# Kernel tuning notes

Measured on AMD Instinct MI355X. Metric: run time of the kernel, lower is better.

The kernel has to match this reference:

```python
import jax, jax.numpy as jnp
import numpy as np

N_E = 1024
E_DIM = 256
N_TOK = 131072


def setup_inputs() -> dict:
    key = jax.random.key(0)
    kz, kw = jax.random.split(key)
    z = jax.random.normal(kz, (N_TOK, E_DIM), dtype=jnp.float32)
    weight = jax.random.normal(kw, (N_E, E_DIM), dtype=jnp.float32)
    return {"z": z, "weight": weight}


def reference(z, weight):
    # squared L2 distances: ||z||^2 + ||e||^2 - 2 z e^T  -> [N, n_e]
    d = (jnp.sum(z * z, axis=1, keepdims=True)
         + jnp.sum(weight * weight, axis=1)
         - 2.0 * jnp.matmul(z, weight.T))
    idx = jnp.argmin(d, axis=1)                       # [N]
    # gather codebook rows instead of materializing the one-hot @ weight matmul
    z_q = weight[idx]                                 # [N, e_dim]
    # straight-through estimator
    z_q = z + jax.lax.stop_gradient(z_q - z)
    # e_mean = mean of one-hot encodings == normalized code counts
    counts = jax.ops.segment_sum(jnp.ones_like(idx, dtype=z.dtype), idx,
                                 num_segments=N_E)    # [n_e]
    e_mean = counts / z.shape[0]
    perplexity = jnp.exp(-jnp.sum(e_mean * jnp.log(e_mean + 1e-10)))
    return z_q, perplexity
```

## Files before the change

### kernel.cpp

```cpp
#include <hip/hip_runtime.h>
#include <math.h>

#define NE   1024
#define ED   256
#define NT   131072
#define SLOTS 32

#define THR_REL 0.016f
#define THR_ABS 0.02f

typedef __attribute__((ext_vector_type(8))) short short8;
typedef __attribute__((ext_vector_type(4))) float f32x4;

__device__ inline unsigned short f2bf(float f) {
    unsigned u = __float_as_uint(f);
    unsigned r = (u + 0x7FFFu + ((u >> 16) & 1u)) >> 16;
    return (unsigned short)r;
}

__device__ inline void gl_lds16(const void* g, void* l) {
    __builtin_amdgcn_global_load_lds(
        (const __attribute__((address_space(1))) unsigned int*)g,
        (__attribute__((address_space(3))) unsigned int*)l, 16, 0, 0);
}

__device__ inline unsigned pack_cand(float s, int code) {
    float qf = (s + 1024.f) * 16.f;
    int q = (int)qf;
    q = q < 0 ? 0 : (q > 65535 ? 65535 : q);
    return ((unsigned)q << 16) | (unsigned)code;
}


__global__ __launch_bounds__(256) void vq_prep(const float* __restrict__ w,
                                               float* __restrict__ wnorm,
                                               int* __restrict__ counts,
                                               unsigned short* __restrict__ wb) {
    int c = blockIdx.x * 256 + threadIdx.x;
    if (c < NE) {
        const float4* row = reinterpret_cast<const float4*>(w + (size_t)c * ED);
        ushort4* wbr = reinterpret_cast<ushort4*>(wb + (size_t)c * ED);
        float s = 0.f;
#pragma unroll 8
        for (int i = 0; i < ED / 4; ++i) {
            float4 v = row[i];
            s += v.x * v.x + v.y * v.y + v.z * v.z + v.w * v.w;
            ushort4 o;
            o.x = f2bf(-2.f * v.x); o.y = f2bf(-2.f * v.y);
            o.z = f2bf(-2.f * v.z); o.w = f2bf(-2.f * v.w);
            wbr[i] = o;
        }
        wnorm[c] = s;
        counts[c] = 0;
    }
}

__global__ __launch_bounds__(1024) void vq_wmax(const float* __restrict__ wnorm,
                                                float* __restrict__ wmax) {
    __shared__ float red[16];
    int tid = threadIdx.x;
    float v = wnorm[tid];
#pragma unroll
    for (int m = 32; m >= 1; m >>= 1) v = fmaxf(v, __shfl_xor(v, m, 64));
    if ((tid & 63) == 0) red[tid >> 6] = v;
    __syncthreads();
    if (tid == 0) {
        float m = red[0];
#pragma unroll
        for (int i = 1; i < 16; ++i) m = fmaxf(m, red[i]);
        wmax[0] = sqrtf(m);
    }
}

__global__ __launch_bounds__(256) void vq_score8(const float* __restrict__ z,
                                                 const unsigned short* __restrict__ wb,
                                                 const float* __restrict__ wnorm,
                                                 const float* __restrict__ wmaxp,
                                                 unsigned* __restrict__ cnt,
                                                 unsigned* __restrict__ cand) {
    __shared__ __align__(16) unsigned short wlds[2][16384];
    __shared__ float wn_lds[NE];
    __shared__ float thr_lds[4][32];

    const int tid  = threadIdx.x;
    const int lane = tid & 63;
    const int wv_  = tid >> 6;
    const int l15  = lane & 15;
    const int l4   = lane >> 4;
    const int row0 = blockIdx.x * 128 + wv_ * 32;

#pragma unroll
    for (int p = 0; p < 8; ++p) {
        int s  = wv_ * 8 + p;
        int nj = s >> 3, kg = s & 7;
        gl_lds16(wb + (size_t)(nj * 16 + l15) * ED + kg * 32 + l4 * 8,
                 &wlds[0][s * 512]);
    }
#pragma unroll
    for (int p = 0; p < 8; ++p) {
        int s  = wv_ * 8 + p;
        int nj = s >> 3, kg = s & 7;
        gl_lds16(wb + (size_t)(64 + nj * 16 + l15) * ED + kg * 32 + l4 * 8,
                 &wlds[1][s * 512]);
    }

    reinterpret_cast<float4*>(wn_lds)[tid] = reinterpret_cast<const float4*>(wnorm)[tid];

    short8 a[2][8];
    float zn2[2];
#pragma unroll
    for (int mi = 0; mi < 2; ++mi) {
        const float* zr = z + (size_t)(row0 + mi * 16 + l15) * ED;
        float s = 0.f;
#pragma unroll
        for (int kg = 0; kg < 8; ++kg) {
            int k0 = kg * 32 + l4 * 8;
            float4 p = *reinterpret_cast<const float4*>(zr + k0);
            float4 q = *reinterpret_cast<const float4*>(zr + k0 + 4);
            s += p.x * p.x + p.y * p.y + p.z * p.z + p.w * p.w
               + q.x * q.x + q.y * q.y + q.z * q.z + q.w * q.w;
            short8 t;
            t[0] = (short)f2bf(p.x); t[1] = (short)f2bf(p.y);
            t[2] = (short)f2bf(p.z); t[3] = (short)f2bf(p.w);
            t[4] = (short)f2bf(q.x); t[5] = (short)f2bf(q.y);
            t[6] = (short)f2bf(q.z); t[7] = (short)f2bf(q.w);
            a[mi][kg] = t;
        }
        zn2[mi] = s;
    }
#pragma unroll
    for (int mi = 0; mi < 2; ++mi) {
        zn2[mi] += __shfl_xor(zn2[mi], 16, 64);
        zn2[mi] += __shfl_xor(zn2[mi], 32, 64);
    }
    float wmax = wmaxp[0];
#pragma unroll
    for (int mi = 0; mi < 2; ++mi)
        thr_lds[wv_][mi * 16 + l15] = THR_REL * sqrtf(zn2[mi]) * wmax + THR_ABS;

    asm volatile("s_waitcnt vmcnt(0) lgkmcnt(0)" ::: "memory");
    __builtin_amdgcn_s_barrier();

    float thrR[2], mn[2];
    int cnt_reg[2];
#pragma unroll
    for (int mi = 0; mi < 2; ++mi) {
        thrR[mi] = thr_lds[wv_][mi * 16 + l15];
        mn[mi] = 3.4e38f;
        cnt_reg[mi] = 0;
    }

    for (int st = 0; st < 16; ++st) {
        const int b  = st & 1;
        const int c0 = st * 64;

        if (st < 15) {
            asm volatile("s_waitcnt vmcnt(8)" ::: "memory");
        } else {
            asm volatile("s_waitcnt vmcnt(0)" ::: "memory");
        }
        __builtin_amdgcn_s_barrier();

        for (int base = 0; base < 4; base += 2) {
            f32x4 acc[2][2];
#pragma unroll
            for (int tb = 0; tb < 2; ++tb) {
                float4 wnv = *reinterpret_cast<const float4*>(
                    &wn_lds[c0 + (base + tb) * 16 + l4 * 4]);
                acc[tb][0] = {wnv.x, wnv.y, wnv.z, wnv.w};
                acc[tb][1] = {wnv.x, wnv.y, wnv.z, wnv.w};
            }

#pragma unroll
            for (int tb = 0; tb < 2; ++tb)
#pragma unroll
                for (int kg = 0; kg < 8; ++kg) {
                    short8 wf = *reinterpret_cast<const short8*>(
                        &wlds[b][(((base + tb) * 8 + kg) * 512) + lane * 8]);
                    acc[tb][0] = __builtin_amdgcn_mfma_f32_16x16x32_bf16(wf, a[0][kg], acc[tb][0], 0, 0, 0);
                    acc[tb][1] = __builtin_amdgcn_mfma_f32_16x16x32_bf16(wf, a[1][kg], acc[tb][1], 0, 0, 0);
                }

            float tmin[2] = {3.4e38f, 3.4e38f};
#pragma unroll
            for (int tb = 0; tb < 2; ++tb)
#pragma unroll
                for (int mi = 0; mi < 2; ++mi)
#pragma unroll
                    for (int r = 0; r < 4; ++r)
                        tmin[mi] = fminf(tmin[mi], acc[tb][mi][r]);
#pragma unroll
            for (int mi = 0; mi < 2; ++mi) {
                float v = tmin[mi];
                v = fminf(v, __shfl_xor(v, 16, 64));
                v = fminf(v, __shfl_xor(v, 32, 64));
                mn[mi] = fminf(mn[mi], v);
            }

            unsigned km[2] = {0u, 0u};
#pragma unroll
            for (int tb = 0; tb < 2; ++tb)
#pragma unroll
                for (int mi = 0; mi < 2; ++mi)
#pragma unroll
                    for (int r = 0; r < 4; ++r)
                        if (acc[tb][mi][r] <= mn[mi] + thrR[mi])
                            km[mi] |= 1u << (tb * 4 + r);

            if (__any((km[0] | km[1]) != 0u)) {
#pragma unroll
                for (int mi = 0; mi < 2; ++mi) {
                    int kc = __popc(km[mi]);
                    int b2 = __shfl_xor(kc, 16, 64);
                    int c2 = __shfl_xor(kc, 32, 64);
                    int d2 = __shfl_xor(b2, 32, 64);
                    int tot = kc + b2 + c2 + d2;
                    if (tot > 0) {
                        int pfx = (l4 == 1) ? b2
                                : (l4 == 2) ? (c2 + d2)
                                : (l4 == 3) ? (b2 + c2 + d2) : 0;
                        int tok = row0 + mi * 16 + l15;
                        int o = 0;
#pragma unroll
                        for (int tb = 0; tb < 2; ++tb)
#pragma unroll
                            for (int r = 0; r < 4; ++r)
                                if (km[mi] & (1u << (tb * 4 + r))) {
                                    int pos = cnt_reg[mi] + pfx + o;
                                    if (pos < SLOTS)
                                        cand[(size_t)tok * SLOTS + pos] =
                                            pack_cand(acc[tb][mi][r],
                                                      c0 + (base + tb) * 16 + l4 * 4 + r);
                                    ++o;
                                }
                        cnt_reg[mi] += tot;
                    }
                }
            }
        }

        asm volatile("s_waitcnt lgkmcnt(0)" ::: "memory");
        __builtin_amdgcn_s_barrier();
        if (st + 2 < 16) {
            const int cN = (st + 2) * 64;
#pragma unroll
            for (int p = 0; p < 8; ++p) {
                int s  = wv_ * 8 + p;
                int nj = s >> 3, kg = s & 7;
                gl_lds16(wb + (size_t)(cN + nj * 16 + l15) * ED + kg * 32 + l4 * 8,
                         &wlds[b][s * 512]);
            }
        }
    }

    if (l4 == 0) {
#pragma unroll
        for (int mi = 0; mi < 2; ++mi) {
            unsigned n = (unsigned)cnt_reg[mi];
            if (n > 255u) n = 255u;
            unsigned marg = (unsigned)(16.f * thrR[mi]) + 2u;
            cnt[row0 + mi * 16 + l15] = n | (marg << 8);
        }
    }
}

__global__ __launch_bounds__(256) void vq_refine(const float* __restrict__ z,
                                                 const float* __restrict__ w,
                                                 const float* __restrict__ wnorm,
                                                 const unsigned* __restrict__ cnt,
                                                 const unsigned* __restrict__ cand,
                                                 int* __restrict__ counts,
                                                 float* __restrict__ out) {
    const int lane = threadIdx.x & 63;
    const int t = blockIdx.x * 4 + (threadIdx.x >> 6);

    const unsigned tpack = cnt[t];
    const unsigned n     = tpack & 0xFFu;
    const unsigned margin = tpack >> 8;

    int bj = NE;
    bool need_exact = true;
    unsigned pk = 0xFFFFFFFFu;
    unsigned long long mask = 0ull;

    if (n >= 1u && n <= (unsigned)SLOTS) {
        if (lane < (int)n) pk = cand[(size_t)t * SLOTS + lane];
        unsigned pmin = pk;
#pragma unroll
        for (int m = 1; m < 64; m <<= 1) {
            unsigned o = __shfl_xor(pmin, m, 64);
            pmin = o < pmin ? o : pmin;
        }
        unsigned qmin = pmin >> 16;
        bool keep = (lane < (int)n) && ((pk >> 16) <= qmin + margin);
        mask = __ballot(keep);
        if (__popcll(mask) == 1) {
            int c = __ffsll(mask) - 1;
            bj = (int)(__shfl(pk, c, 64) & 0xFFFFu);
            need_exact = false;
        }
    }

    if (need_exact) {
        float4 zv = reinterpret_cast<const float4*>(z + (size_t)t * ED)[lane];
        float bs = 3.4e38f;
        bj = NE;
        if (n >= 1u && n <= (unsigned)SLOTS) {
            unsigned long long m2 = mask;
            while (m2) {
                int c = __ffsll(m2) - 1;
                m2 &= m2 - 1;
                int j = (int)(__shfl(pk, c, 64) & 0xFFFFu);
                float4 wv = reinterpret_cast<const float4*>(w + (size_t)j * ED)[lane];
                float d = fmaf(zv.x, wv.x, fmaf(zv.y, wv.y, fmaf(zv.z, wv.z, zv.w * wv.w)));
#pragma unroll
                for (int m = 1; m < 64; m <<= 1) d += __shfl_xor(d, m, 64);
                float s = fmaf(-2.f, d, wnorm[j]);
                if (s < bs || (s == bs && j < bj)) { bs = s; bj = j; }
            }
        } else {
            for (int j = 0; j < NE; ++j) {
                float4 wv = reinterpret_cast<const float4*>(w + (size_t)j * ED)[lane];
                float d = fmaf(zv.x, wv.x, fmaf(zv.y, wv.y, fmaf(zv.z, wv.z, zv.w * wv.w)));
#pragma unroll
                for (int m = 1; m < 64; m <<= 1) d += __shfl_xor(d, m, 64);
                float s = fmaf(-2.f, d, wnorm[j]);
                if (s < bs || (s == bs && j < bj)) { bs = s; bj = j; }
            }
        }
    }

    float4 bw = reinterpret_cast<const float4*>(w + (size_t)bj * ED)[lane];
    reinterpret_cast<float4*>(out + (size_t)t * ED)[lane] = bw;
    if (lane == 0) atomicAdd(&counts[bj], 1);
}

__global__ __launch_bounds__(1024) void vq_pplx(const int* __restrict__ counts,
                                                float* __restrict__ out) {
    __shared__ float red[16];
    int tid = threadIdx.x;
    float e = (float)counts[tid] * (1.0f / (float)NT);
    float t = -e * logf(e + 1e-10f);
#pragma unroll
    for (int m = 32; m >= 1; m >>= 1) t += __shfl_down(t, m, 64);
    if ((tid & 63) == 0) red[tid >> 6] = t;
    __syncthreads();
    if (tid < 16) {
        float s = red[tid];
#pragma unroll
        for (int m = 8; m >= 1; m >>= 1) s += __shfl_down(s, m, 16);
        if (tid == 0) out[(size_t)NT * ED] = expf(s);
    }
}

#define TM 64
#define TN 64
#define KC 64

__global__ __launch_bounds__(256) void vq_prep0(const float* __restrict__ w,
                                                float* __restrict__ wnorm,
                                                int* __restrict__ counts) {
    int c = blockIdx.x * blockDim.x + threadIdx.x;
    if (c < NE) {
        const float4* row = reinterpret_cast<const float4*>(w + (size_t)c * ED);
        float s = 0.f;
#pragma unroll 8
        for (int i = 0; i < ED / 4; ++i) {
            float4 v = row[i];
            s += v.x * v.x + v.y * v.y + v.z * v.z + v.w * v.w;
        }
        wnorm[c] = s;
        counts[c] = 0;
    }
}

__global__ __launch_bounds__(256) void vq_argmin0(const float* __restrict__ z,
                                                  const float* __restrict__ w,
                                                  const float* __restrict__ wnorm,
                                                  int* __restrict__ idx_out,
                                                  int* __restrict__ counts) {
    __shared__ float zs[ED][TM];
    __shared__ float wsh[KC][TN];
    const int tid  = threadIdx.x;
    const int row0 = blockIdx.x * TM;
    const int cg   = tid & 15;
    const int tg   = tid >> 4;
#pragma unroll
    for (int p = 0; p < 16; ++p) {
        int f = p * 256 + tid;
        int k = f >> 4;
        int g = f & 15;
        float4 v;
        v.x = z[(size_t)(row0 + g * 4 + 0) * ED + k];
        v.y = z[(size_t)(row0 + g * 4 + 1) * ED + k];
        v.z = z[(size_t)(row0 + g * 4 + 2) * ED + k];
        v.w = z[(size_t)(row0 + g * 4 + 3) * ED + k];
        *reinterpret_cast<float4*>(&zs[k][g * 4]) = v;
    }
    float best[4];
    int   bidx[4];
#pragma unroll
    for (int i = 0; i < 4; ++i) { best[i] = 3.4e38f; bidx[i] = 0; }
    for (int ct = 0; ct < NE / TN; ++ct) {
        const int c0 = ct * TN;
        float acc[4][4];
#pragma unroll
        for (int i = 0; i < 4; ++i)
#pragma unroll
            for (int j = 0; j < 4; ++j) acc[i][j] = 0.f;
        for (int kc = 0; kc < ED / KC; ++kc) {
            __syncthreads();
#pragma unroll
            for (int p = 0; p < 4; ++p) {
                int f = p * 256 + tid;
                int k = f >> 4;
                int g = f & 15;
                float4 v;
                v.x = w[(size_t)(c0 + g * 4 + 0) * ED + kc * KC + k];
                v.y = w[(size_t)(c0 + g * 4 + 1) * ED + kc * KC + k];
                v.z = w[(size_t)(c0 + g * 4 + 2) * ED + kc * KC + k];
                v.w = w[(size_t)(c0 + g * 4 + 3) * ED + kc * KC + k];
                *reinterpret_cast<float4*>(&wsh[k][g * 4]) = v;
            }
            __syncthreads();
#pragma unroll 8
            for (int k = 0; k < KC; ++k) {
                float4 zv = *reinterpret_cast<const float4*>(&zs[kc * KC + k][tg * 4]);
                float4 wv = *reinterpret_cast<const float4*>(&wsh[k][cg * 4]);
                float zr[4] = { zv.x, zv.y, zv.z, zv.w };
                float wr[4] = { wv.x, wv.y, wv.z, wv.w };
#pragma unroll
                for (int i = 0; i < 4; ++i)
#pragma unroll
                    for (int j = 0; j < 4; ++j)
                        acc[i][j] = fmaf(zr[i], wr[j], acc[i][j]);
            }
        }
#pragma unroll
        for (int j = 0; j < 4; ++j) {
            int c = c0 + cg * 4 + j;
            float wn = wnorm[c];
#pragma unroll
            for (int i = 0; i < 4; ++i) {
                float s = fmaf(-2.f, acc[i][j], wn);
                if (s < best[i]) { best[i] = s; bidx[i] = c; }
            }
        }
    }
#pragma unroll
    for (int m = 1; m < 16; m <<= 1) {
#pragma unroll
        for (int i = 0; i < 4; ++i) {
            float ov = __shfl_xor(best[i], m, 64);
            int   oi = __shfl_xor(bidx[i], m, 64);
            if (ov < best[i] || (ov == best[i] && oi < bidx[i])) {
                best[i] = ov; bidx[i] = oi;
            }
        }
    }
    if (cg == 0) {
#pragma unroll
        for (int i = 0; i < 4; ++i) {
            int t = row0 + tg * 4 + i;
            idx_out[t] = bidx[i];
            atomicAdd(&counts[bidx[i]], 1);
        }
    }
}

__global__ __launch_bounds__(256) void vq_gather0(const float* __restrict__ w,
                                                  const int* __restrict__ idx,
                                                  float* __restrict__ out) {
    int tid = threadIdx.x;
    int t   = blockIdx.x * 4 + (tid >> 6);
    int c4  = tid & 63;
    int id  = idx[t];
    float4 v = reinterpret_cast<const float4*>(w + (size_t)id * ED)[c4];
    reinterpret_cast<float4*>(out + (size_t)t * ED)[c4] = v;
}

extern "C" void kernel_launch(void* const* d_in, const int* in_sizes, int n_in,
                              void* d_out, int out_size, void* d_ws, size_t ws_size,
                              hipStream_t stream) {
    const float* z = (const float*)d_in[0];
    const float* w = (const float*)d_in[1];
    float* out = (float*)d_out;
    char* ws = (char*)d_ws;

    float*          wnorm  = (float*)ws;
    int*            counts = (int*)(ws + 4096);
    float*          wmax   = (float*)(ws + 8192);
    unsigned short* wb     = (unsigned short*)(ws + 8448);
    unsigned*       cnt    = (unsigned*)(ws + 532736);
    unsigned*       cand   = (unsigned*)(ws + 1057024);
    const size_t need = 1057024 + (size_t)NT * SLOTS * 4;

    if (ws_size >= need) {
        vq_prep<<<4, 256, 0, stream>>>(w, wnorm, counts, wb);
        vq_wmax<<<1, 1024, 0, stream>>>(wnorm, wmax);
        vq_score8<<<NT / 128, 256, 0, stream>>>(z, wb, wnorm, wmax, cnt, cand);
        vq_refine<<<NT / 4, 256, 0, stream>>>(z, w, wnorm, cnt, cand, counts, out);
        vq_pplx<<<1, 1024, 0, stream>>>(counts, out);
    } else {
        int* idxw = (int*)(ws + 8192);
        vq_prep0<<<(NE + 255) / 256, 256, 0, stream>>>(w, wnorm, counts);
        vq_argmin0<<<NT / TM, 256, 0, stream>>>(z, w, wnorm, idxw, counts);
        vq_gather0<<<NT / 4, 256, 0, stream>>>(w, idxw, out);
        vq_pplx<<<1, 1024, 0, stream>>>(counts, out);
    }
}
```

Before: 275.7 us.

## Fuse codebook max-norm into prep via atomicMax and unroll full 64-code stage

Removes the separate vq_wmax launch by having vq_prep compute the max squared codebook norm with an atomicMax on the float bit pattern, after a memset of the slot. In the scoring kernel, per-token thresholds stay in registers instead of going through LDS. The stage loop now runs all four 16-code tiles at once (eight accumulators) and raises wave priority around the MFMA block. The candidate threshold and extraction run once per 64 codes instead of per 32, which cuts shuffles and branches but raises register pressure. The memset adds a small operation in place of the removed kernel.

```diff
diff --git a/kernel.cpp b/kernel.cpp
--- a/kernel.cpp
+++ b/kernel.cpp
@@ -35,7 +35,8 @@
 __global__ __launch_bounds__(256) void vq_prep(const float* __restrict__ w,
                                                float* __restrict__ wnorm,
                                                int* __restrict__ counts,
-                                               unsigned short* __restrict__ wb) {
+                                               unsigned short* __restrict__ wb,
+                                               unsigned* __restrict__ wmaxsq) {
     int c = blockIdx.x * 256 + threadIdx.x;
     if (c < NE) {
         const float4* row = reinterpret_cast<const float4*>(w + (size_t)c * ED);
@@ -52,35 +53,18 @@
         }
         wnorm[c] = s;
         counts[c] = 0;
-    }
-}
-
-__global__ __launch_bounds__(1024) void vq_wmax(const float* __restrict__ wnorm,
-                                                float* __restrict__ wmax) {
-    __shared__ float red[16];
-    int tid = threadIdx.x;
-    float v = wnorm[tid];
-#pragma unroll
-    for (int m = 32; m >= 1; m >>= 1) v = fmaxf(v, __shfl_xor(v, m, 64));
-    if ((tid & 63) == 0) red[tid >> 6] = v;
-    __syncthreads();
-    if (tid == 0) {
-        float m = red[0];
-#pragma unroll
-        for (int i = 1; i < 16; ++i) m = fmaxf(m, red[i]);
-        wmax[0] = sqrtf(m);
-    }
-}
-
-__global__ __launch_bounds__(256) void vq_score8(const float* __restrict__ z,
+        atomicMax(wmaxsq, __float_as_uint(s));
+    }
+}
+
+__global__ __launch_bounds__(256) void vq_score9(const float* __restrict__ z,
                                                  const unsigned short* __restrict__ wb,
                                                  const float* __restrict__ wnorm,
-                                                 const float* __restrict__ wmaxp,
+                                                 const unsigned* __restrict__ wmaxsq,
                                                  unsigned* __restrict__ cnt,
                                                  unsigned* __restrict__ cand) {
     __shared__ __align__(16) unsigned short wlds[2][16384];
     __shared__ float wn_lds[NE];
-    __shared__ float thr_lds[4][32];
 
     const int tid  = threadIdx.x;
     const int lane = tid & 63;
@@ -107,48 +91,38 @@
     reinterpret_cast<float4*>(wn_lds)[tid] = reinterpret_cast<const float4*>(wnorm)[tid];
 
     short8 a[2][8];
-    float zn2[2];
-#pragma unroll
-    for (int mi = 0; mi < 2; ++mi) {
-        const float* zr = z + (size_t)(row0 + mi * 16 + l15) * ED;
-        float s = 0.f;
-#pragma unroll
-        for (int kg = 0; kg < 8; ++kg) {
-            int k0 = kg * 32 + l4 * 8;
-            float4 p = *reinterpret_cast<const float4*>(zr + k0);
-            float4 q = *reinterpret_cast<const float4*>(zr + k0 + 4);
-            s += p.x * p.x + p.y * p.y + p.z * p.z + p.w * p.w
-               + q.x * q.x + q.y * q.y + q.z * q.z + q.w * q.w;
-            short8 t;
-            t[0] = (short)f2bf(p.x); t[1] = (short)f2bf(p.y);
-            t[2] = (short)f2bf(p.z); t[3] = (short)f2bf(p.w);
-            t[4] = (short)f2bf(q.x); t[5] = (short)f2bf(q.y);
-            t[6] = (short)f2bf(q.z); t[7] = (short)f2bf(q.w);
-            a[mi][kg] = t;
-        }
-        zn2[mi] = s;
-    }
-#pragma unroll
-    for (int mi = 0; mi < 2; ++mi) {
-        zn2[mi] += __shfl_xor(zn2[mi], 16, 64);
-        zn2[mi] += __shfl_xor(zn2[mi], 32, 64);
-    }
-    float wmax = wmaxp[0];
-#pragma unroll
-    for (int mi = 0; mi < 2; ++mi)
-        thr_lds[wv_][mi * 16 + l15] = THR_REL * sqrtf(zn2[mi]) * wmax + THR_ABS;
+    float thrR[2], mn[2];
+    int cnt_reg[2];
+    {
+        float wmax = sqrtf(__uint_as_float(wmaxsq[0]));
+#pragma unroll
+        for (int mi = 0; mi < 2; ++mi) {
+            const float* zr = z + (size_t)(row0 + mi * 16 + l15) * ED;
+            float s = 0.f;
+#pragma unroll
+            for (int kg = 0; kg < 8; ++kg) {
+                int k0 = kg * 32 + l4 * 8;
+                float4 p = *reinterpret_cast<const float4*>(zr + k0);
+                float4 q = *reinterpret_cast<const float4*>(zr + k0 + 4);
+                s += p.x * p.x + p.y * p.y + p.z * p.z + p.w * p.w
+                   + q.x * q.x + q.y * q.y + q.z * q.z + q.w * q.w;
+                short8 t;
+                t[0] = (short)f2bf(p.x); t[1] = (short)f2bf(p.y);
+                t[2] = (short)f2bf(p.z); t[3] = (short)f2bf(p.w);
+                t[4] = (short)f2bf(q.x); t[5] = (short)f2bf(q.y);
+                t[6] = (short)f2bf(q.z); t[7] = (short)f2bf(q.w);
+                a[mi][kg] = t;
+            }
+            s += __shfl_xor(s, 16, 64);
+            s += __shfl_xor(s, 32, 64);
+            thrR[mi] = THR_REL * sqrtf(s) * wmax + THR_ABS;
+            mn[mi] = 3.4e38f;
+            cnt_reg[mi] = 0;
+        }
+    }
 
     asm volatile("s_waitcnt vmcnt(0) lgkmcnt(0)" ::: "memory");
     __builtin_amdgcn_s_barrier();
-
-    float thrR[2], mn[2];
-    int cnt_reg[2];
-#pragma unroll
-    for (int mi = 0; mi < 2; ++mi) {
-        thrR[mi] = thr_lds[wv_][mi * 16 + l15];
-        mn[mi] = 3.4e38f;
-        cnt_reg[mi] = 0;
-    }
 
     for (int st = 0; st < 16; ++st) {
         const int b  = st & 1;
@@ -161,80 +135,114 @@
         }
         __builtin_amdgcn_s_barrier();
 
-        for (int base = 0; base < 4; base += 2) {
-            f32x4 acc[2][2];
-#pragma unroll
-            for (int tb = 0; tb < 2; ++tb) {
-                float4 wnv = *reinterpret_cast<const float4*>(
-                    &wn_lds[c0 + (base + tb) * 16 + l4 * 4]);
-                acc[tb][0] = {wnv.x, wnv.y, wnv.z, wnv.w};
-                acc[tb][1] = {wnv.x, wnv.y, wnv.z, wnv.w};
-            }
-
-#pragma unroll
-            for (int tb = 0; tb < 2; ++tb)
-#pragma unroll
-                for (int kg = 0; kg < 8; ++kg) {
-                    short8 wf = *reinterpret_cast<const short8*>(
-                        &wlds[b][(((base + tb) * 8 + kg) * 512) + lane * 8]);
-                    acc[tb][0] = __builtin_amdgcn_mfma_f32_16x16x32_bf16(wf, a[0][kg], acc[tb][0], 0, 0, 0);
-                    acc[tb][1] = __builtin_amdgcn_mfma_f32_16x16x32_bf16(wf, a[1][kg], acc[tb][1], 0, 0, 0);
-                }
-
-            float tmin[2] = {3.4e38f, 3.4e38f};
-#pragma unroll
-            for (int tb = 0; tb < 2; ++tb)
-#pragma unroll
-                for (int mi = 0; mi < 2; ++mi)
-#pragma unroll
-                    for (int r = 0; r < 4; ++r)
-                        tmin[mi] = fminf(tmin[mi], acc[tb][mi][r]);
+        f32x4 acc0A, acc0B, acc1A, acc1B, acc2A, acc2B, acc3A, acc3B;
+        {
+            float4 w0 = *reinterpret_cast<const float4*>(&wn_lds[c0 + 0 * 16 + l4 * 4]);
+            float4 w1 = *reinterpret_cast<const float4*>(&wn_lds[c0 + 1 * 16 + l4 * 4]);
+            float4 w2 = *reinterpret_cast<const float4*>(&wn_lds[c0 + 2 * 16 + l4 * 4]);
+            float4 w3 = *reinterpret_cast<const float4*>(&wn_lds[c0 + 3 * 16 + l4 * 4]);
+            acc0A = {w0.x, w0.y, w0.z, w0.w}; acc0B = acc0A;
+            acc1A = {w1.x, w1.y, w1.z, w1.w}; acc1B = acc1A;
+            acc2A = {w2.x, w2.y, w2.z, w2.w}; acc2B = acc2A;
+            acc3A = {w3.x, w3.y, w3.z, w3.w}; acc3B = acc3A;
+        }
+
+        __builtin_amdgcn_s_setprio(1);
+#pragma unroll
+        for (int kg = 0; kg < 8; ++kg) {
+            short8 wf0 = *reinterpret_cast<const short8*>(
+                &wlds[b][((0 * 8 + kg) * 512) + lane * 8]);
+            acc0A = __builtin_amdgcn_mfma_f32_16x16x32_bf16(wf0, a[0][kg], acc0A, 0, 0, 0);
+            acc0B = __builtin_amdgcn_mfma_f32_16x16x32_bf16(wf0, a[1][kg], acc0B, 0, 0, 0);
+            short8 wf1 = *reinterpret_cast<const short8*>(
+                &wlds[b][((1 * 8 + kg) * 512) + lane * 8]);
+            acc1A = __builtin_amdgcn_mfma_f32_16x16x32_bf16(wf1, a[0][kg], acc1A, 0, 0, 0);
+            acc1B = __builtin_amdgcn_mfma_f32_16x16x32_bf16(wf1, a[1][kg], acc1B, 0, 0, 0);
+            short8 wf2 = *reinterpret_cast<const short8*>(
+                &wlds[b][((2 * 8 + kg) * 512) + lane * 8]);
+            acc2A = __builtin_amdgcn_mfma_f32_16x16x32_bf16(wf2, a[0][kg], acc2A, 0, 0, 0);
+            acc2B = __builtin_amdgcn_mfma_f32_16x16x32_bf16(wf2, a[1][kg], acc2B, 0, 0, 0);
+            short8 wf3 = *reinterpret_cast<const short8*>(
+                &wlds[b][((3 * 8 + kg) * 512) + lane * 8]);
+            acc3A = __builtin_amdgcn_mfma_f32_16x16x32_bf16(wf3, a[0][kg], acc3A, 0, 0, 0);
+            acc3B = __builtin_amdgcn_mfma_f32_16x16x32_bf16(wf3, a[1][kg], acc3B, 0, 0, 0);
+        }
+        __builtin_amdgcn_s_setprio(0);
+
+        float tmin[2];
+        {
+            f32x4 m0 = acc0A, m1 = acc1A;
+#pragma unroll
+            for (int r = 0; r < 4; ++r) {
+                m0[r] = fminf(m0[r], acc2A[r]);
+                m1[r] = fminf(m1[r], acc3A[r]);
+            }
+            float v = fminf(fminf(m0[0], m0[1]), fminf(m0[2], m0[3]));
+            v = fminf(v, fminf(fminf(m1[0], m1[1]), fminf(m1[2], m1[3])));
+            tmin[0] = v;
+            f32x4 n0 = acc0B, n1 = acc1B;
+#pragma unroll
+            for (int r = 0; r < 4; ++r) {
+                n0[r] = fminf(n0[r], acc2B[r]);
+                n1[r] = fminf(n1[r], acc3B[r]);
+            }
+            float u = fminf(fminf(n0[0], n0[1]), fminf(n0[2], n0[3]));
+            u = fminf(u, fminf(fminf(n1[0], n1[1]), fminf(n1[2], n1[3])));
+            tmin[1] = u;
+        }
+#pragma unroll
+        for (int mi = 0; mi < 2; ++mi) {
+            float v = tmin[mi];
+            v = fminf(v, __shfl_xor(v, 16, 64));
+            v = fminf(v, __shfl_xor(v, 32, 64));
+            mn[mi] = fminf(mn[mi], v);
+        }
+
+        unsigned km[2] = {0u, 0u};
+#pragma unroll
+        for (int r = 0; r < 4; ++r) {
+            if (acc0A[r] <= mn[0] + thrR[0]) km[0] |= 1u << (0 + r);
+            if (acc1A[r] <= mn[0] + thrR[0]) km[0] |= 1u << (4 + r);
+            if (acc2A[r] <= mn[0] + thrR[0]) km[0] |= 1u << (8 + r);
+            if (acc3A[r] <= mn[0] + thrR[0]) km[0] |= 1u << (12 + r);
+            if (acc0B[r] <= mn[1] + thrR[1]) km[1] |= 1u << (0 + r);
+            if (acc1B[r] <= mn[1] + thrR[1]) km[1] |= 1u << (4 + r);
+            if (acc2B[r] <= mn[1] + thrR[1]) km[1] |= 1u << (8 + r);
+            if (acc3B[r] <= mn[1] + thrR[1]) km[1] |= 1u << (12 + r);
+        }
+
+        if (__any((km[0] | km[1]) != 0u)) {
 #pragma unroll
             for (int mi = 0; mi < 2; ++mi) {
-                float v = tmin[mi];
-                v = fminf(v, __shfl_xor(v, 16, 64));
-                v = fminf(v, __shfl_xor(v, 32, 64));
-                mn[mi] = fminf(mn[mi], v);
-            }
-
-            unsigned km[2] = {0u, 0u};
-#pragma unroll
-            for (int tb = 0; tb < 2; ++tb)
-#pragma unroll
-                for (int mi = 0; mi < 2; ++mi)
-#pragma unroll
-                    for (int r = 0; r < 4; ++r)
-                        if (acc[tb][mi][r] <= mn[mi] + thrR[mi])
-                            km[mi] |= 1u << (tb * 4 + r);
-
-            if (__any((km[0] | km[1]) != 0u)) {
-#pragma unroll
-                for (int mi = 0; mi < 2; ++mi) {
-                    int kc = __popc(km[mi]);
-                    int b2 = __shfl_xor(kc, 16, 64);
-                    int c2 = __shfl_xor(kc, 32, 64);
-                    int d2 = __shfl_xor(b2, 32, 64);
-                    int tot = kc + b2 + c2 + d2;
-                    if (tot > 0) {
-                        int pfx = (l4 == 1) ? b2
-                                : (l4 == 2) ? (c2 + d2)
-                                : (l4 == 3) ? (b2 + c2 + d2) : 0;
-                        int tok = row0 + mi * 16 + l15;
-                        int o = 0;
-#pragma unroll
-                        for (int tb = 0; tb < 2; ++tb)
-#pragma unroll
-                            for (int r = 0; r < 4; ++r)
-                                if (km[mi] & (1u << (tb * 4 + r))) {
-                                    int pos = cnt_reg[mi] + pfx + o;
-                                    if (pos < SLOTS)
-                                        cand[(size_t)tok * SLOTS + pos] =
-                                            pack_cand(acc[tb][mi][r],
-                                                      c0 + (base + tb) * 16 + l4 * 4 + r);
-                                    ++o;
-                                }
-                        cnt_reg[mi] += tot;
-                    }
+                int kc = __popc(km[mi]);
+                int b2 = __shfl_xor(kc, 16, 64);
+                int c2 = __shfl_xor(kc, 32, 64);
+                int d2 = __shfl_xor(b2, 32, 64);
+                int tot = kc + b2 + c2 + d2;
+                if (tot > 0) {
+                    int pfx = (l4 == 1) ? b2
+                            : (l4 == 2) ? (c2 + d2)
+                            : (l4 == 3) ? (b2 + c2 + d2) : 0;
+                    int tok = row0 + mi * 16 + l15;
+                    int o = 0;
+                    const f32x4* accs[4] = {
+                        mi == 0 ? &acc0A : &acc0B,
+                        mi == 0 ? &acc1A : &acc1B,
+                        mi == 0 ? &acc2A : &acc2B,
+                        mi == 0 ? &acc3A : &acc3B };
+#pragma unroll
+                    for (int t = 0; t < 4; ++t)
+#pragma unroll
+                        for (int r = 0; r < 4; ++r)
+                            if (km[mi] & (1u << (t * 4 + r))) {
+                                int pos = cnt_reg[mi] + pfx + o;
+                                if (pos < SLOTS)
+                                    cand[(size_t)tok * SLOTS + pos] =
+                                        pack_cand((*accs[t])[r],
+                                                  c0 + t * 16 + l4 * 4 + r);
+                                ++o;
+                            }
+                    cnt_reg[mi] += tot;
                 }
             }
         }
@@ -489,16 +497,16 @@
 
     float*          wnorm  = (float*)ws;
     int*            counts = (int*)(ws + 4096);
-    float*          wmax   = (float*)(ws + 8192);
+    unsigned*       wmaxsq = (unsigned*)(ws + 8192);
     unsigned short* wb     = (unsigned short*)(ws + 8448);
     unsigned*       cnt    = (unsigned*)(ws + 532736);
     unsigned*       cand   = (unsigned*)(ws + 1057024);
     const size_t need = 1057024 + (size_t)NT * SLOTS * 4;
 
     if (ws_size >= need) {
-        vq_prep<<<4, 256, 0, stream>>>(w, wnorm, counts, wb);
-        vq_wmax<<<1, 1024, 0, stream>>>(wnorm, wmax);
-        vq_score8<<<NT / 128, 256, 0, stream>>>(z, wb, wnorm, wmax, cnt, cand);
+        hipMemsetAsync(wmaxsq, 0, 4, stream);
+        vq_prep<<<4, 256, 0, stream>>>(w, wnorm, counts, wb, wmaxsq);
+        vq_score9<<<NT / 128, 256, 0, stream>>>(z, wb, wnorm, wmaxsq, cnt, cand);
         vq_refine<<<NT / 4, 256, 0, stream>>>(z, w, wnorm, cnt, cand, counts, out);
         vq_pplx<<<1, 1024, 0, stream>>>(counts, out);
     } else {
```

Result: faster. 260.3 us (-5.6%).
